# Optimization experiments

Measured on AMD Instinct MI355X. Metric: run time of the kernel, lower is better.

The kernel has to match this reference:

```python
import jax, jax.numpy as jnp
import numpy as np

# Haar (db1) decomposition filters, pywt convention
_S = 1.0 / np.sqrt(2.0)
# dec_lo = [s, s], dec_hi = [-s, s]. Each scalar input v becomes signal [v, 0]
# (zero-pad to 2**dwt_level = 2). The single valid DWT coeff (mode='zero') is
#   cA = v * dec_lo[1] = v * s ;  cD = v * dec_hi[1] = v * s
CA_COEF = np.float32(_S)   # dec_lo[1]
CD_COEF = np.float32(_S)   # dec_hi[1]

B, N, F, OUT = 8, 20000, 256, 256
WAVELET_FULL_LEN = 2  # len(cA) + len(cD) for level-1 db1 on length-2 signal


def setup_inputs() -> dict:
    key = jax.random.key(0)
    kx, kw, kb, kwo, kbo = jax.random.split(key, 5)
    x = jax.random.normal(kx, (B, N, F), dtype=jnp.float32)
    # per-feature nn.Linear(wavelet_full_len, 1) stacked: weight [F, 2], bias [F]
    lim_nl = 1.0 / np.sqrt(WAVELET_FULL_LEN)
    W_nl = jax.random.uniform(kw, (F, WAVELET_FULL_LEN), jnp.float32, -lim_nl, lim_nl)
    b_nl = jax.random.uniform(kb, (F,), jnp.float32, -lim_nl, lim_nl)
    # linear_out: [out_dim, feat_dim] torch layout, bias [out_dim]
    lim_o = 1.0 / np.sqrt(F)
    W_out = jax.random.uniform(kwo, (OUT, F), jnp.float32, -lim_o, lim_o)
    b_out = jax.random.uniform(kbo, (OUT,), jnp.float32, -lim_o, lim_o)
    return {"x": x, "W_nl": W_nl, "b_nl": b_nl, "W_out": W_out, "b_out": b_out}


def reference(x, W_nl, b_nl, W_out, b_out):
    # Batched wavelet features: for each scalar, coeffs are [cA, cD] = [s*v, s*v]
    # feat_wave: [B, N, F, 2]
    feat_wave = jnp.stack([x * CA_COEF, x * CD_COEF], axis=-1)
    # Per-feature Linear(2, 1), batched over the feature dim
    agg_nl = jnp.einsum("bnfk,fk->bnf", feat_wave, W_nl) + b_nl  # [B, N, F]
    # Output linear (dropout is identity in eval)
    out = jnp.einsum("bnf,of->bno", agg_nl, W_out) + b_out  # [B, N, OUT]
    return out
```

## Files before the change

### kernel.cpp

```cpp
#include <hip/hip_runtime.h>

typedef __bf16 bf16x8 __attribute__((ext_vector_type(8)));
typedef float f32x4 __attribute__((ext_vector_type(4)));
typedef unsigned short ushort8 __attribute__((ext_vector_type(8)));

__device__ __forceinline__ unsigned short f2b(float f) {
    unsigned int u = __float_as_uint(f);
    return (unsigned short)((u + 0x7fffu + ((u >> 16) & 1u)) >> 16);
}

__global__ __launch_bounds__(256) void wk_prep(
    const float* __restrict__ Wnl, const float* __restrict__ bnl,
    const float* __restrict__ Wout, const float* __restrict__ bout,
    unsigned short* __restrict__ wfrag, float* __restrict__ wbias) {
    int b = blockIdx.x, tid = threadIdx.x;
    if (b < 256) {
        int t = b * 256 + tid;
        int j = t & 7;
        int lane = (t >> 3) & 63;
        int ks = (t >> 9) & 7;
        int ct = t >> 12;
        int f = ks * 32 + ((lane >> 4) << 3) + j;
        int o = ct * 16 + (lane & 15);
        float c = 0.70710678f * (Wnl[2 * f] + Wnl[2 * f + 1]);
        wfrag[t] = f2b(c * Wout[o * 256 + f]);
    } else {
        int o = tid;
        float s = 0.f;
        #pragma unroll 8
        for (int f = 0; f < 256; ++f) s += bnl[f] * Wout[o * 256 + f];
        wbias[o] = bout[o] + s;
    }
}

__global__ __launch_bounds__(512, 2) void wk_main(
    const float* __restrict__ x, const unsigned short* __restrict__ wfrag,
    const float* __restrict__ wbias, float* __restrict__ out) {
    const int tid  = threadIdx.x;
    const int lane = tid & 63;
    const int w    = tid >> 6;
    const int m    = lane & 15;
    const int quad = lane >> 4;

    const int half    = blockIdx.x & 1;
    const int rowTile = blockIdx.x >> 1;
    const int r0      = rowTile * 128 + w * 16;

    __shared__ bf16x8 Wlds[4096];

    {
        int4* dst = (int4*)Wlds;
        const int4* src = (const int4*)(wfrag + half * 32768);
        #pragma unroll
        for (int i = 0; i < 8; ++i) dst[tid + i * 512] = src[tid + i * 512];
    }

    const float4* xv = (const float4*)(x + (size_t)(r0 + m) * 256);
    const int kb = quad * 2;
    float4 a0[8], a1[8];
    #pragma unroll
    for (int ks = 0; ks < 8; ++ks) {
        a0[ks] = xv[ks * 8 + kb];
        a1[ks] = xv[ks * 8 + kb + 1];
    }

    float bias_r[8];
    #pragma unroll
    for (int ct = 0; ct < 8; ++ct)
        bias_r[ct] = wbias[half * 128 + ct * 16 + m];

    bf16x8 afr[8];
    #pragma unroll
    for (int ks = 0; ks < 8; ++ks) {
        ushort8 s;
        s[0] = f2b(a0[ks].x); s[1] = f2b(a0[ks].y);
        s[2] = f2b(a0[ks].z); s[3] = f2b(a0[ks].w);
        s[4] = f2b(a1[ks].x); s[5] = f2b(a1[ks].y);
        s[6] = f2b(a1[ks].z); s[7] = f2b(a1[ks].w);
        afr[ks] = __builtin_bit_cast(bf16x8, s);
    }

    __syncthreads();

    #pragma unroll
    for (int ct = 0; ct < 8; ++ct) {
        f32x4 acc = {bias_r[ct], bias_r[ct], bias_r[ct], bias_r[ct]};
        #pragma unroll
        for (int ks = 0; ks < 8; ++ks) {
            acc = __builtin_amdgcn_mfma_f32_16x16x32_bf16(
                afr[ks], Wlds[(ct * 8 + ks) * 64 + lane], acc, 0, 0, 0);
        }
        size_t base = (size_t)(r0 + quad * 4) * 256 + half * 128 + ct * 16 + m;
        out[base]       = acc[0];
        out[base + 256] = acc[1];
        out[base + 512] = acc[2];
        out[base + 768] = acc[3];
    }
}

extern "C" void kernel_launch(void* const* d_in, const int* in_sizes, int n_in,
                              void* d_out, int out_size, void* d_ws, size_t ws_size,
                              hipStream_t stream) {
    const float* x    = (const float*)d_in[0];
    const float* Wnl  = (const float*)d_in[1];
    const float* bnl  = (const float*)d_in[2];
    const float* Wout = (const float*)d_in[3];
    const float* bout = (const float*)d_in[4];

    unsigned short* wfrag = (unsigned short*)d_ws;
    float* wbias = (float*)((char*)d_ws + 131072);

    wk_prep<<<257, 256, 0, stream>>>(Wnl, bnl, Wout, bout, wfrag, wbias);
    wk_main<<<2500, 512, 0, stream>>>(x, wfrag, wbias, (float*)d_out);
}
```

Measured before the change: 305.8 us.

## Compute all output columns per block, reusing the x fragment across two weight halves

New measurement: 300.6 us. Within noise of the previous version (-1.7%).

```diff
diff --git a/kernel.cpp b/kernel.cpp
--- a/kernel.cpp
+++ b/kernel.cpp
@@ -33,7 +33,7 @@
     }
 }
 
-__global__ __launch_bounds__(512, 2) void wk_main(
+__global__ __launch_bounds__(512, 4) void wk_main(
     const float* __restrict__ x, const unsigned short* __restrict__ wfrag,
     const float* __restrict__ wbias, float* __restrict__ out) {
     const int tid  = threadIdx.x;
@@ -41,60 +41,66 @@
     const int w    = tid >> 6;
     const int m    = lane & 15;
     const int quad = lane >> 4;
-
-    const int half    = blockIdx.x & 1;
-    const int rowTile = blockIdx.x >> 1;
-    const int r0      = rowTile * 128 + w * 16;
+    const int r0   = blockIdx.x * 128 + w * 16;
 
     __shared__ bf16x8 Wlds[4096];
 
     {
         int4* dst = (int4*)Wlds;
-        const int4* src = (const int4*)(wfrag + half * 32768);
+        const int4* src = (const int4*)wfrag;
         #pragma unroll
         for (int i = 0; i < 8; ++i) dst[tid + i * 512] = src[tid + i * 512];
     }
 
     const float4* xv = (const float4*)(x + (size_t)(r0 + m) * 256);
-    const int kb = quad * 2;
-    float4 a0[8], a1[8];
-    #pragma unroll
-    for (int ks = 0; ks < 8; ++ks) {
-        a0[ks] = xv[ks * 8 + kb];
-        a1[ks] = xv[ks * 8 + kb + 1];
-    }
-
-    float bias_r[8];
-    #pragma unroll
-    for (int ct = 0; ct < 8; ++ct)
-        bias_r[ct] = wbias[half * 128 + ct * 16 + m];
-
     bf16x8 afr[8];
     #pragma unroll
-    for (int ks = 0; ks < 8; ++ks) {
-        ushort8 s;
-        s[0] = f2b(a0[ks].x); s[1] = f2b(a0[ks].y);
-        s[2] = f2b(a0[ks].z); s[3] = f2b(a0[ks].w);
-        s[4] = f2b(a1[ks].x); s[5] = f2b(a1[ks].y);
-        s[6] = f2b(a1[ks].z); s[7] = f2b(a1[ks].w);
-        afr[ks] = __builtin_bit_cast(bf16x8, s);
+    for (int c = 0; c < 2; ++c) {
+        float4 u[4], v[4];
+        #pragma unroll
+        for (int q = 0; q < 4; ++q) {
+            int ks = c * 4 + q;
+            u[q] = xv[ks * 8 + quad * 2];
+            v[q] = xv[ks * 8 + quad * 2 + 1];
+        }
+        #pragma unroll
+        for (int q = 0; q < 4; ++q) {
+            ushort8 s;
+            s[0] = f2b(u[q].x); s[1] = f2b(u[q].y);
+            s[2] = f2b(u[q].z); s[3] = f2b(u[q].w);
+            s[4] = f2b(v[q].x); s[5] = f2b(v[q].y);
+            s[6] = f2b(v[q].z); s[7] = f2b(v[q].w);
+            afr[c * 4 + q] = __builtin_bit_cast(bf16x8, s);
+        }
     }
 
     __syncthreads();
 
     #pragma unroll
-    for (int ct = 0; ct < 8; ++ct) {
-        f32x4 acc = {bias_r[ct], bias_r[ct], bias_r[ct], bias_r[ct]};
+    for (int h = 0; h < 2; ++h) {
+        if (h == 1) {
+            __syncthreads();
+            int4* dst = (int4*)Wlds;
+            const int4* src = (const int4*)(wfrag + 32768);
+            #pragma unroll
+            for (int i = 0; i < 8; ++i) dst[tid + i * 512] = src[tid + i * 512];
+            __syncthreads();
+        }
         #pragma unroll
-        for (int ks = 0; ks < 8; ++ks) {
-            acc = __builtin_amdgcn_mfma_f32_16x16x32_bf16(
-                afr[ks], Wlds[(ct * 8 + ks) * 64 + lane], acc, 0, 0, 0);
+        for (int ct = 0; ct < 8; ++ct) {
+            float b = wbias[h * 128 + ct * 16 + m];
+            f32x4 acc = {b, b, b, b};
+            #pragma unroll
+            for (int ks = 0; ks < 8; ++ks) {
+                acc = __builtin_amdgcn_mfma_f32_16x16x32_bf16(
+                    afr[ks], Wlds[(ct * 8 + ks) * 64 + lane], acc, 0, 0, 0);
+            }
+            size_t base = (size_t)(r0 + quad * 4) * 256 + h * 128 + ct * 16 + m;
+            out[base]       = acc[0];
+            out[base + 256] = acc[1];
+            out[base + 512] = acc[2];
+            out[base + 768] = acc[3];
         }
-        size_t base = (size_t)(r0 + quad * 4) * 256 + half * 128 + ct * 16 + m;
-        out[base]       = acc[0];
-        out[base + 256] = acc[1];
-        out[base + 512] = acc[2];
-        out[base + 768] = acc[3];
     }
 }
 
@@ -111,5 +117,5 @@
     float* wbias = (float*)((char*)d_ws + 131072);
 
     wk_prep<<<257, 256, 0, stream>>>(Wnl, bnl, Wout, bout, wfrag, wbias);
-    wk_main<<<2500, 512, 0, stream>>>(x, wfrag, wbias, (float*)d_out);
+    wk_main<<<1250, 512, 0, stream>>>(x, wfrag, wbias, (float*)d_out);
 }
```

## Use persistent blocks with full-weight LDS and register-prefetched row tiles

Applied to the files above, without the earlier changes.

Result: slower. 580.1 us (+89.7%).

```diff
diff --git a/kernel.cpp b/kernel.cpp
--- a/kernel.cpp
+++ b/kernel.cpp
@@ -33,7 +33,7 @@
     }
 }
 
-__global__ __launch_bounds__(512, 2) void wk_main(
+__global__ __launch_bounds__(512) void wk_main(
     const float* __restrict__ x, const unsigned short* __restrict__ wfrag,
     const float* __restrict__ wbias, float* __restrict__ out) {
     const int tid  = threadIdx.x;
@@ -42,59 +42,72 @@
     const int m    = lane & 15;
     const int quad = lane >> 4;
 
-    const int half    = blockIdx.x & 1;
-    const int rowTile = blockIdx.x >> 1;
-    const int r0      = rowTile * 128 + w * 16;
-
-    __shared__ bf16x8 Wlds[4096];
+    __shared__ bf16x8 Wlds[8192];
 
     {
         int4* dst = (int4*)Wlds;
-        const int4* src = (const int4*)(wfrag + half * 32768);
+        const int4* src = (const int4*)wfrag;
         #pragma unroll
-        for (int i = 0; i < 8; ++i) dst[tid + i * 512] = src[tid + i * 512];
+        for (int i = 0; i < 16; ++i) dst[tid + i * 512] = src[tid + i * 512];
     }
 
-    const float4* xv = (const float4*)(x + (size_t)(r0 + m) * 256);
-    const int kb = quad * 2;
-    float4 a0[8], a1[8];
+    float bias_r[16];
     #pragma unroll
-    for (int ks = 0; ks < 8; ++ks) {
-        a0[ks] = xv[ks * 8 + kb];
-        a1[ks] = xv[ks * 8 + kb + 1];
-    }
-
-    float bias_r[8];
-    #pragma unroll
-    for (int ct = 0; ct < 8; ++ct)
-        bias_r[ct] = wbias[half * 128 + ct * 16 + m];
-
-    bf16x8 afr[8];
-    #pragma unroll
-    for (int ks = 0; ks < 8; ++ks) {
-        ushort8 s;
-        s[0] = f2b(a0[ks].x); s[1] = f2b(a0[ks].y);
-        s[2] = f2b(a0[ks].z); s[3] = f2b(a0[ks].w);
-        s[4] = f2b(a1[ks].x); s[5] = f2b(a1[ks].y);
-        s[6] = f2b(a1[ks].z); s[7] = f2b(a1[ks].w);
-        afr[ks] = __builtin_bit_cast(bf16x8, s);
-    }
+    for (int ct = 0; ct < 16; ++ct) bias_r[ct] = wbias[ct * 16 + m];
 
     __syncthreads();
 
-    #pragma unroll
-    for (int ct = 0; ct < 8; ++ct) {
-        f32x4 acc = {bias_r[ct], bias_r[ct], bias_r[ct], bias_r[ct]};
+    const int NT = 10000;
+    const int stride = 2048;
+    int t = blockIdx.x * 8 + w;
+
+    float4 raw[16];
+    {
+        const float4* xv = (const float4*)(x) + (size_t)t * 1024 + m * 64 + quad * 2;
         #pragma unroll
         for (int ks = 0; ks < 8; ++ks) {
-            acc = __builtin_amdgcn_mfma_f32_16x16x32_bf16(
-                afr[ks], Wlds[(ct * 8 + ks) * 64 + lane], acc, 0, 0, 0);
+            raw[2 * ks]     = xv[ks * 8];
+            raw[2 * ks + 1] = xv[ks * 8 + 1];
         }
-        size_t base = (size_t)(r0 + quad * 4) * 256 + half * 128 + ct * 16 + m;
-        out[base]       = acc[0];
-        out[base + 256] = acc[1];
-        out[base + 512] = acc[2];
-        out[base + 768] = acc[3];
+    }
+
+    while (t < NT) {
+        bf16x8 afr[8];
+        #pragma unroll
+        for (int ks = 0; ks < 8; ++ks) {
+            float4 u = raw[2 * ks], v = raw[2 * ks + 1];
+            ushort8 s;
+            s[0] = f2b(u.x); s[1] = f2b(u.y); s[2] = f2b(u.z); s[3] = f2b(u.w);
+            s[4] = f2b(v.x); s[5] = f2b(v.y); s[6] = f2b(v.z); s[7] = f2b(v.w);
+            afr[ks] = __builtin_bit_cast(bf16x8, s);
+        }
+
+        int tn = t + stride;
+        if (tn < NT) {
+            const float4* xv = (const float4*)(x) + (size_t)tn * 1024 + m * 64 + quad * 2;
+            #pragma unroll
+            for (int ks = 0; ks < 8; ++ks) {
+                raw[2 * ks]     = xv[ks * 8];
+                raw[2 * ks + 1] = xv[ks * 8 + 1];
+            }
+        }
+
+        size_t rbase = ((size_t)t * 16 + quad * 4) * 256;
+        #pragma unroll
+        for (int ct = 0; ct < 16; ++ct) {
+            f32x4 acc = {bias_r[ct], bias_r[ct], bias_r[ct], bias_r[ct]};
+            #pragma unroll
+            for (int ks = 0; ks < 8; ++ks) {
+                acc = __builtin_amdgcn_mfma_f32_16x16x32_bf16(
+                    afr[ks], Wlds[(ct * 8 + ks) * 64 + lane], acc, 0, 0, 0);
+            }
+            size_t base = rbase + ct * 16 + m;
+            out[base]       = acc[0];
+            out[base + 256] = acc[1];
+            out[base + 512] = acc[2];
+            out[base + 768] = acc[3];
+        }
+        t = tn;
     }
 }
 
@@ -111,5 +124,5 @@
     float* wbias = (float*)((char*)d_ws + 131072);
 
     wk_prep<<<257, 256, 0, stream>>>(Wnl, bnl, Wout, bout, wfrag, wbias);
-    wk_main<<<2500, 512, 0, stream>>>(x, wfrag, wbias, (float*)d_out);
+    wk_main<<<256, 512, 0, stream>>>(x, wfrag, wbias, (float*)d_out);
 }
```
